# Performance work log

Measured on AMD Instinct MI355X. Metric: run time of the kernel, lower is better.

## Reference

```python
import jax, jax.numpy as jnp
import numpy as np

WIN = 9  # window size per spatial dim (default [9,9,9] for 3D)


def _window_sum(x):
    # Depthwise conv with an all-ones [9,9,9] kernel, stride 1, zero pad 4
    # == sliding-window box sum. lax.reduce_window is the efficient, exact form.
    pad = WIN // 2
    return jax.lax.reduce_window(
        x, 0.0, jax.lax.add,
        window_dimensions=(1, 1, WIN, WIN, WIN),
        window_strides=(1, 1, 1, 1, 1),
        padding=((0, 0), (0, 0), (pad, pad), (pad, pad), (pad, pad)),
    )


def setup_inputs() -> dict:
    key = jax.random.key(0)
    k1, k2 = jax.random.split(key)
    shape = (2, 1, 160, 160, 160)  # [B, C, D, H, W]
    y_true = jax.random.normal(k1, shape, dtype=jnp.float32)
    y_pred = jax.random.normal(k2, shape, dtype=jnp.float32)
    return {"y_true": y_true, "y_pred": y_pred}


def reference(y_true, y_pred):
    Ii, Ji = y_true, y_pred
    win_size = jnp.asarray(WIN ** 3, dtype=Ii.dtype)  # 729

    I2 = Ii * Ii
    J2 = Ji * Ji
    IJ = Ii * Ji

    I_sum = _window_sum(Ii)
    J_sum = _window_sum(Ji)
    I2_sum = _window_sum(I2)
    J2_sum = _window_sum(J2)
    IJ_sum = _window_sum(IJ)

    u_I = I_sum / win_size
    u_J = J_sum / win_size

    cross = IJ_sum - u_J * I_sum - u_I * J_sum + u_I * u_J * win_size
    I_var = I2_sum - 2.0 * u_I * I_sum + u_I * u_I * win_size
    J_var = J2_sum - 2.0 * u_J * J_sum + u_J * u_J * win_size

    cc = cross * cross / (I_var * J_var + 1e-05)
    # mean over spatial dims [2,3,4] -> [B,C], then mean -> scalar
    return (1.0 - jnp.mean(cc, axis=(2, 3, 4))).mean()
```

## Files before the change

### kernel.cpp

```cpp
#include <hip/hip_runtime.h>


typedef float floatx2 __attribute__((ext_vector_type(2)));

constexpr int W = 160, H = 160, D = 160;
constexpr int SLICE = W * H;
constexpr int NVOX  = W * H * D;
constexpr int BATCH = 2;
constexpr int FROW  = 5 * W;
constexpr float RW  = 1.0f / 729.0f;

constexpr int TPB_Z = 256;
constexpr int XG4   = W / 4;
constexpr int CHZ   = 8, NCHZ = D / CHZ;
constexpr int NTH_Z = BATCH * XG4 * H * NCHZ;
constexpr int NBLK_Z = NTH_Z / TPB_Z;

constexpr int TPB_YX = 256;
constexpr int XG  = W / 8;
constexpr int CHY = 4, NCHY = H / CHY;
constexpr int NTUP = BATCH * D * NCHY;
constexpr int TPW  = 3;
constexpr int TPBLK = 4 * TPW;
constexpr int NBLK_YX = (NTUP + TPBLK - 1) / TPBLK;

__device__ inline unsigned int pk4(float a, float b, float c, float d) {
    unsigned int u = 0;
    u = __builtin_amdgcn_cvt_pk_fp8_f32(a, b, u, false);
    u = __builtin_amdgcn_cvt_pk_fp8_f32(c, d, u, true);
    return u;
}
__device__ inline void up8(uint2 v, float* o) {
    floatx2 t;
    t = __builtin_amdgcn_cvt_pk_f32_fp8(v.x, false); o[0] = t[0]; o[1] = t[1];
    t = __builtin_amdgcn_cvt_pk_f32_fp8(v.x, true);  o[2] = t[0]; o[3] = t[1];
    t = __builtin_amdgcn_cvt_pk_f32_fp8(v.y, false); o[4] = t[0]; o[5] = t[1];
    t = __builtin_amdgcn_cvt_pk_f32_fp8(v.y, true);  o[6] = t[0]; o[7] = t[1];
}

__global__ __launch_bounds__(TPB_Z) void pass_z(const float* __restrict__ I,
                                                const float* __restrict__ J,
                                                unsigned char* __restrict__ outA) {
    int t = blockIdx.x * TPB_Z + threadIdx.x;
    int xg = t % XG4;
    int y  = (t / XG4) % H;
    int c  = (t / (XG4 * H)) % NCHZ;
    int b  = t / (XG4 * H * NCHZ);
    int x0 = xg * 4;
    const float* Ib = I + (size_t)b * NVOX + y * W + x0;
    const float* Jb = J + (size_t)b * NVOX + y * W + x0;
    unsigned char* ob = outA + ((size_t)b * D * H + y) * FROW + x0;

    float s[5][4];
#pragma unroll
    for (int f = 0; f < 5; ++f)
#pragma unroll
        for (int i = 0; i < 4; ++i) s[f][i] = 0.f;

    auto addS = [&](int zz) {
        float4 a = *(const float4*)(Ib + (size_t)zz * SLICE);
        float4 bb = *(const float4*)(Jb + (size_t)zz * SLICE);
        float av[4] = {a.x, a.y, a.z, a.w};
        float bv[4] = {bb.x, bb.y, bb.z, bb.w};
#pragma unroll
        for (int i = 0; i < 4; ++i) {
            float x = av[i], yv = bv[i];
            s[0][i] += x; s[1][i] += yv;
            s[2][i] += x * x; s[3][i] += yv * yv; s[4][i] += x * yv;
        }
    };

    int z0 = c * CHZ;
    for (int zz = (z0 - 4 < 0 ? 0 : z0 - 4); zz <= z0 + 4; ++zz) addS(zz);

#pragma unroll
    for (int dz = 0; dz < CHZ; ++dz) {
        int z = z0 + dz;
        int za = z + 5, zs = z - 4;
        bool ha = za < D, hs = zs >= 0;
        float4 Az = ha ? *(const float4*)(Ib + (size_t)za * SLICE) : make_float4(0.f, 0.f, 0.f, 0.f);
        float4 Bz = ha ? *(const float4*)(Jb + (size_t)za * SLICE) : make_float4(0.f, 0.f, 0.f, 0.f);
        float4 As = hs ? *(const float4*)(Ib + (size_t)zs * SLICE) : make_float4(0.f, 0.f, 0.f, 0.f);
        float4 Bs = hs ? *(const float4*)(Jb + (size_t)zs * SLICE) : make_float4(0.f, 0.f, 0.f, 0.f);

        unsigned char* op = ob + (size_t)z * (H * FROW);
#pragma unroll
        for (int f = 0; f < 5; ++f)
            *(unsigned int*)(op + f * W) = pk4(s[f][0], s[f][1], s[f][2], s[f][3]);

        float ae[4] = {Az.x, Az.y, Az.z, Az.w};
        float be[4] = {Bz.x, Bz.y, Bz.z, Bz.w};
        float al[4] = {As.x, As.y, As.z, As.w};
        float bl[4] = {Bs.x, Bs.y, Bs.z, Bs.w};
#pragma unroll
        for (int i = 0; i < 4; ++i) {
            s[0][i] += ae[i] - al[i];
            s[1][i] += be[i] - bl[i];
            s[2][i] += ae[i] * ae[i] - al[i] * al[i];
            s[3][i] += be[i] * be[i] - bl[i] * bl[i];
            s[4][i] += ae[i] * be[i] - al[i] * bl[i];
        }
    }
}

__global__ __launch_bounds__(TPB_YX) void pass_yx(const unsigned char* __restrict__ A,
                                                  double* __restrict__ partials) {
    int tid = threadIdx.x;
    int lane = tid & 63, wvi = tid >> 6;
    int g = lane / XG, xg = lane % XG;
    int tuple = blockIdx.x * TPBLK + wvi * TPW + g;
    bool valid = (g < TPW) && (tuple < NTUP);
    int t = valid ? tuple : 0;
    int yc = t % NCHY;
    int z  = (t / NCHY) % D;
    int b  = t / (NCHY * D);
    int x0 = xg * 8;
    const unsigned char* __restrict__ base =
        A + (size_t)(b * D + z) * H * FROW + x0;
    int y0 = yc * CHY;

    float s[5][8];
#pragma unroll
    for (int f = 0; f < 5; ++f)
#pragma unroll
        for (int i = 0; i < 8; ++i) s[f][i] = 0.f;

    int ylo = y0 - 4 < 0 ? 0 : y0 - 4;
    int yhi = y0 + 4 > H - 1 ? H - 1 : y0 + 4;
    for (int yy = ylo; yy <= yhi; ++yy) {
        const unsigned char* rp = base + (size_t)yy * FROW;
#pragma unroll
        for (int f = 0; f < 5; ++f) {
            uint2 v = *(const uint2*)(rp + f * W);
            float u[8]; up8(v, u);
#pragma unroll
            for (int i = 0; i < 8; ++i) s[f][i] += u[i];
        }
    }

    double acc = 0.0;
#pragma unroll
    for (int dy = 0; dy < CHY; ++dy) {
        int ye = y0 + dy + 5, yl = y0 + dy - 4;
        bool he = ye < H, hl = yl >= 0;
        uint2 pe[5], pl[5];
        const unsigned char* pre = base + (size_t)(he ? ye : 0) * FROW;
        const unsigned char* prl = base + (size_t)(hl ? yl : 0) * FROW;
#pragma unroll
        for (int f = 0; f < 5; ++f) {
            pe[f] = he ? *(const uint2*)(pre + f * W) : make_uint2(0u, 0u);
            pl[f] = hl ? *(const uint2*)(prl + f * W) : make_uint2(0u, 0u);
        }

        float wv5[5][8];
#pragma unroll
        for (int f = 0; f < 5; ++f) {
            float p0 = s[f][0];
            float p1 = p0 + s[f][1];
            float p2 = p1 + s[f][2];
            float p3 = p2 + s[f][3];
            float p4 = p3 + s[f][4];
            float p5 = p4 + s[f][5];
            float p6 = p5 + s[f][6];
            float tot = p6 + s[f][7];
            float a0 = tot - p3, a1 = tot - p4, a2 = tot - p5, a3 = tot - p6;
            float L0 = __shfl_up(a0, 1), L1 = __shfl_up(a1, 1);
            float L2 = __shfl_up(a2, 1), L3 = __shfl_up(a3, 1);
            float R0 = __shfl_down(p0, 1), R1 = __shfl_down(p1, 1);
            float R2 = __shfl_down(p2, 1), R3 = __shfl_down(p3, 1);
            if (xg == 0)      { L0 = 0.f; L1 = 0.f; L2 = 0.f; L3 = 0.f; }
            if (xg == XG - 1) { R0 = 0.f; R1 = 0.f; R2 = 0.f; R3 = 0.f; }
            wv5[f][0] = L0 + p4;
            wv5[f][1] = L1 + p5;
            wv5[f][2] = L2 + p6;
            wv5[f][3] = L3 + tot;
            wv5[f][4] = tot + R0;
            wv5[f][5] = (tot - p0) + R1;
            wv5[f][6] = (tot - p1) + R2;
            wv5[f][7] = (tot - p2) + R3;
        }

        float rowcc = 0.f;
#pragma unroll
        for (int i = 0; i < 8; ++i) {
            float Is = wv5[0][i], Js = wv5[1][i];
            float I2s = wv5[2][i], J2s = wv5[3][i], IJs = wv5[4][i];
            float tI = RW * Is;
            float cross = __builtin_fmaf(-tI, Js, IJs);
            float Iv    = __builtin_fmaf(-tI, Is, I2s);
            float Jv    = __builtin_fmaf(-(RW * Js), Js, J2s);
            float den   = __builtin_fmaf(Iv, Jv, 1e-5f);
            rowcc = __builtin_fmaf(cross * cross, __builtin_amdgcn_rcpf(den), rowcc);
        }
        acc += (double)rowcc;

#pragma unroll
        for (int f = 0; f < 5; ++f) {
            float ue[8], ul[8];
            up8(pe[f], ue); up8(pl[f], ul);
#pragma unroll
            for (int i = 0; i < 8; ++i) s[f][i] += ue[i] - ul[i];
        }
    }

    if (!valid) acc = 0.0;

#pragma unroll
    for (int off = 32; off > 0; off >>= 1) acc += __shfl_down(acc, off);
    __shared__ double sm[TPB_YX / 64];
    if ((tid & 63) == 0) sm[tid >> 6] = acc;
    __syncthreads();
    if (tid == 0) {
        double tt = 0.0;
#pragma unroll
        for (int i = 0; i < TPB_YX / 64; ++i) tt += sm[i];
        partials[blockIdx.x] = tt;
    }
}

__global__ __launch_bounds__(256) void finalize(const double* __restrict__ p,
                                                float* __restrict__ out) {
    double v = 0.0;
    for (int i = threadIdx.x; i < NBLK_YX; i += 256) v += p[i];
#pragma unroll
    for (int off = 32; off > 0; off >>= 1) v += __shfl_down(v, off);
    __shared__ double sm[4];
    int lane = threadIdx.x & 63, wid = threadIdx.x >> 6;
    if (lane == 0) sm[wid] = v;
    __syncthreads();
    if (threadIdx.x == 0) {
        double tt = 0.0;
#pragma unroll
        for (int i = 0; i < 4; ++i) tt += sm[i];
        out[0] = (float)(1.0 - tt / (double)((double)BATCH * (double)NVOX));
    }
}

extern "C" void kernel_launch(void* const* d_in, const int* in_sizes, int n_in,
                              void* d_out, int out_size, void* d_ws, size_t ws_size,
                              hipStream_t stream) {
    const float* I = (const float*)d_in[0];
    const float* J = (const float*)d_in[1];
    float* out = (float*)d_out;

    unsigned char* bufA = (unsigned char*)d_ws;
    double* partials = (double*)(bufA + ((size_t)BATCH * 5 * NVOX + 255) / 256 * 256);

    pass_z<<<NBLK_Z, TPB_Z, 0, stream>>>(I, J, bufA);
    pass_yx<<<NBLK_YX, TPB_YX, 0, stream>>>(bufA, partials);
    finalize<<<1, 256, 0, stream>>>(partials, out);
}
```

Before: 68.34 us.

## Move x-window sum into z pass and drop shuffles from y pass

The z pass now loads a 12-wide neighborhood (left, middle, right float4) for each thread, keeps z-running sums over 12 columns, and writes x-windowed sums to the fp8 intermediate. The y pass then only needs the y sliding window, so the cross-lane shuffles and prefix sums go away, and its chunk size drops from 4 to 2 with a simpler one-tuple-per-thread mapping. The aim is cheaper pass_y work and more parallelism. In exchange the z pass reads three times as much input per slice and holds three times as many accumulators, which raises register pressure. The z inner loop is also no longer unrolled.

```diff
diff --git a/kernel.cpp b/kernel.cpp
--- a/kernel.cpp
+++ b/kernel.cpp
@@ -11,18 +11,16 @@
 constexpr float RW  = 1.0f / 729.0f;
 
 constexpr int TPB_Z = 256;
-constexpr int XG4   = W / 4;
+constexpr int XGZ   = W / 4;
 constexpr int CHZ   = 8, NCHZ = D / CHZ;
-constexpr int NTH_Z = BATCH * XG4 * H * NCHZ;
+constexpr int NTH_Z = BATCH * XGZ * H * NCHZ;
 constexpr int NBLK_Z = NTH_Z / TPB_Z;
 
-constexpr int TPB_YX = 256;
-constexpr int XG  = W / 8;
-constexpr int CHY = 4, NCHY = H / CHY;
-constexpr int NTUP = BATCH * D * NCHY;
-constexpr int TPW  = 3;
-constexpr int TPBLK = 4 * TPW;
-constexpr int NBLK_YX = (NTUP + TPBLK - 1) / TPBLK;
+constexpr int TPB_Y = 256;
+constexpr int XGY   = W / 8;
+constexpr int CHY   = 2, NCHY = H / CHY;
+constexpr int NTH_Y = BATCH * D * NCHY * XGY;
+constexpr int NBLK_Y = NTH_Y / TPB_Y;
 
 __device__ inline unsigned int pk4(float a, float b, float c, float d) {
     unsigned int u = 0;
@@ -42,117 +40,63 @@
                                                 const float* __restrict__ J,
                                                 unsigned char* __restrict__ outA) {
     int t = blockIdx.x * TPB_Z + threadIdx.x;
-    int xg = t % XG4;
-    int y  = (t / XG4) % H;
-    int c  = (t / (XG4 * H)) % NCHZ;
-    int b  = t / (XG4 * H * NCHZ);
+    int xg = t % XGZ;
+    int y  = (t / XGZ) % H;
+    int c  = (t / (XGZ * H)) % NCHZ;
+    int b  = t / (XGZ * H * NCHZ);
     int x0 = xg * 4;
     const float* Ib = I + (size_t)b * NVOX + y * W + x0;
     const float* Jb = J + (size_t)b * NVOX + y * W + x0;
-    unsigned char* ob = outA + ((size_t)b * D * H + y) * FROW + x0;
-
-    float s[5][4];
+    bool hasL = xg > 0, hasR = xg < XGZ - 1;
+    const float4 Z4 = make_float4(0.f, 0.f, 0.f, 0.f);
+
+    float s[5][12];
 #pragma unroll
     for (int f = 0; f < 5; ++f)
 #pragma unroll
-        for (int i = 0; i < 4; ++i) s[f][i] = 0.f;
-
-    auto addS = [&](int zz) {
-        float4 a = *(const float4*)(Ib + (size_t)zz * SLICE);
-        float4 bb = *(const float4*)(Jb + (size_t)zz * SLICE);
-        float av[4] = {a.x, a.y, a.z, a.w};
-        float bv[4] = {bb.x, bb.y, bb.z, bb.w};
-#pragma unroll
-        for (int i = 0; i < 4; ++i) {
-            float x = av[i], yv = bv[i];
-            s[0][i] += x; s[1][i] += yv;
-            s[2][i] += x * x; s[3][i] += yv * yv; s[4][i] += x * yv;
+        for (int i = 0; i < 12; ++i) s[f][i] = 0.f;
+
+    auto addT = [&](int zz) {
+        const float* ip = Ib + (size_t)zz * SLICE;
+        const float* jp = Jb + (size_t)zz * SLICE;
+        float4 Li = hasL ? *(const float4*)(ip - 4) : Z4;
+        float4 Mi = *(const float4*)(ip);
+        float4 Ri = hasR ? *(const float4*)(ip + 4) : Z4;
+        float4 Lj = hasL ? *(const float4*)(jp - 4) : Z4;
+        float4 Mj = *(const float4*)(jp);
+        float4 Rj = hasR ? *(const float4*)(jp + 4) : Z4;
+        float a[12] = {Li.x, Li.y, Li.z, Li.w, Mi.x, Mi.y, Mi.z, Mi.w, Ri.x, Ri.y, Ri.z, Ri.w};
+        float bb[12] = {Lj.x, Lj.y, Lj.z, Lj.w, Mj.x, Mj.y, Mj.z, Mj.w, Rj.x, Rj.y, Rj.z, Rj.w};
+#pragma unroll
+        for (int i = 0; i < 12; ++i) {
+            s[0][i] += a[i]; s[1][i] += bb[i];
+            s[2][i] += a[i] * a[i]; s[3][i] += bb[i] * bb[i]; s[4][i] += a[i] * bb[i];
         }
     };
+    auto subT = [&](int zz) {
+        const float* ip = Ib + (size_t)zz * SLICE;
+        const float* jp = Jb + (size_t)zz * SLICE;
+        float4 Li = hasL ? *(const float4*)(ip - 4) : Z4;
+        float4 Mi = *(const float4*)(ip);
+        float4 Ri = hasR ? *(const float4*)(ip + 4) : Z4;
+        float4 Lj = hasL ? *(const float4*)(jp - 4) : Z4;
+        float4 Mj = *(const float4*)(jp);
+        float4 Rj = hasR ? *(const float4*)(jp + 4) : Z4;
+        float a[12] = {Li.x, Li.y, Li.z, Li.w, Mi.x, Mi.y, Mi.z, Mi.w, Ri.x, Ri.y, Ri.z, Ri.w};
+        float bb[12] = {Lj.x, Lj.y, Lj.z, Lj.w, Mj.x, Mj.y, Mj.z, Mj.w, Rj.x, Rj.y, Rj.z, Rj.w};
+#pragma unroll
+        for (int i = 0; i < 12; ++i) {
+            s[0][i] -= a[i]; s[1][i] -= bb[i];
+            s[2][i] -= a[i] * a[i]; s[3][i] -= bb[i] * bb[i]; s[4][i] -= a[i] * bb[i];
+        }
+    };
 
     int z0 = c * CHZ;
-    for (int zz = (z0 - 4 < 0 ? 0 : z0 - 4); zz <= z0 + 4; ++zz) addS(zz);
-
-#pragma unroll
+    for (int zz = (z0 - 4 < 0 ? 0 : z0 - 4); zz <= z0 + 4; ++zz) addT(zz);
+
     for (int dz = 0; dz < CHZ; ++dz) {
         int z = z0 + dz;
-        int za = z + 5, zs = z - 4;
-        bool ha = za < D, hs = zs >= 0;
-        float4 Az = ha ? *(const float4*)(Ib + (size_t)za * SLICE) : make_float4(0.f, 0.f, 0.f, 0.f);
-        float4 Bz = ha ? *(const float4*)(Jb + (size_t)za * SLICE) : make_float4(0.f, 0.f, 0.f, 0.f);
-        float4 As = hs ? *(const float4*)(Ib + (size_t)zs * SLICE) : make_float4(0.f, 0.f, 0.f, 0.f);
-        float4 Bs = hs ? *(const float4*)(Jb + (size_t)zs * SLICE) : make_float4(0.f, 0.f, 0.f, 0.f);
-
-        unsigned char* op = ob + (size_t)z * (H * FROW);
-#pragma unroll
-        for (int f = 0; f < 5; ++f)
-            *(unsigned int*)(op + f * W) = pk4(s[f][0], s[f][1], s[f][2], s[f][3]);
-
-        float ae[4] = {Az.x, Az.y, Az.z, Az.w};
-        float be[4] = {Bz.x, Bz.y, Bz.z, Bz.w};
-        float al[4] = {As.x, As.y, As.z, As.w};
-        float bl[4] = {Bs.x, Bs.y, Bs.z, Bs.w};
-#pragma unroll
-        for (int i = 0; i < 4; ++i) {
-            s[0][i] += ae[i] - al[i];
-            s[1][i] += be[i] - bl[i];
-            s[2][i] += ae[i] * ae[i] - al[i] * al[i];
-            s[3][i] += be[i] * be[i] - bl[i] * bl[i];
-            s[4][i] += ae[i] * be[i] - al[i] * bl[i];
-        }
-    }
-}
-
-__global__ __launch_bounds__(TPB_YX) void pass_yx(const unsigned char* __restrict__ A,
-                                                  double* __restrict__ partials) {
-    int tid = threadIdx.x;
-    int lane = tid & 63, wvi = tid >> 6;
-    int g = lane / XG, xg = lane % XG;
-    int tuple = blockIdx.x * TPBLK + wvi * TPW + g;
-    bool valid = (g < TPW) && (tuple < NTUP);
-    int t = valid ? tuple : 0;
-    int yc = t % NCHY;
-    int z  = (t / NCHY) % D;
-    int b  = t / (NCHY * D);
-    int x0 = xg * 8;
-    const unsigned char* __restrict__ base =
-        A + (size_t)(b * D + z) * H * FROW + x0;
-    int y0 = yc * CHY;
-
-    float s[5][8];
-#pragma unroll
-    for (int f = 0; f < 5; ++f)
-#pragma unroll
-        for (int i = 0; i < 8; ++i) s[f][i] = 0.f;
-
-    int ylo = y0 - 4 < 0 ? 0 : y0 - 4;
-    int yhi = y0 + 4 > H - 1 ? H - 1 : y0 + 4;
-    for (int yy = ylo; yy <= yhi; ++yy) {
-        const unsigned char* rp = base + (size_t)yy * FROW;
-#pragma unroll
-        for (int f = 0; f < 5; ++f) {
-            uint2 v = *(const uint2*)(rp + f * W);
-            float u[8]; up8(v, u);
-#pragma unroll
-            for (int i = 0; i < 8; ++i) s[f][i] += u[i];
-        }
-    }
-
-    double acc = 0.0;
-#pragma unroll
-    for (int dy = 0; dy < CHY; ++dy) {
-        int ye = y0 + dy + 5, yl = y0 + dy - 4;
-        bool he = ye < H, hl = yl >= 0;
-        uint2 pe[5], pl[5];
-        const unsigned char* pre = base + (size_t)(he ? ye : 0) * FROW;
-        const unsigned char* prl = base + (size_t)(hl ? yl : 0) * FROW;
-#pragma unroll
-        for (int f = 0; f < 5; ++f) {
-            pe[f] = he ? *(const uint2*)(pre + f * W) : make_uint2(0u, 0u);
-            pl[f] = hl ? *(const uint2*)(prl + f * W) : make_uint2(0u, 0u);
-        }
-
-        float wv5[5][8];
+        unsigned char* op = outA + ((size_t)(b * D + z) * H + y) * FROW + x0;
 #pragma unroll
         for (int f = 0; f < 5; ++f) {
             float p0 = s[f][0];
@@ -162,29 +106,71 @@
             float p4 = p3 + s[f][4];
             float p5 = p4 + s[f][5];
             float p6 = p5 + s[f][6];
-            float tot = p6 + s[f][7];
-            float a0 = tot - p3, a1 = tot - p4, a2 = tot - p5, a3 = tot - p6;
-            float L0 = __shfl_up(a0, 1), L1 = __shfl_up(a1, 1);
-            float L2 = __shfl_up(a2, 1), L3 = __shfl_up(a3, 1);
-            float R0 = __shfl_down(p0, 1), R1 = __shfl_down(p1, 1);
-            float R2 = __shfl_down(p2, 1), R3 = __shfl_down(p3, 1);
-            if (xg == 0)      { L0 = 0.f; L1 = 0.f; L2 = 0.f; L3 = 0.f; }
-            if (xg == XG - 1) { R0 = 0.f; R1 = 0.f; R2 = 0.f; R3 = 0.f; }
-            wv5[f][0] = L0 + p4;
-            wv5[f][1] = L1 + p5;
-            wv5[f][2] = L2 + p6;
-            wv5[f][3] = L3 + tot;
-            wv5[f][4] = tot + R0;
-            wv5[f][5] = (tot - p0) + R1;
-            wv5[f][6] = (tot - p1) + R2;
-            wv5[f][7] = (tot - p2) + R3;
+            float p7 = p6 + s[f][7];
+            float p8 = p7 + s[f][8];
+            float p9 = p8 + s[f][9];
+            float p10 = p9 + s[f][10];
+            float p11 = p10 + s[f][11];
+            *(unsigned int*)(op + f * W) = pk4(p8, p9 - p0, p10 - p1, p11 - p2);
+        }
+        int za = z + 5, zs = z - 4;
+        if (za < D) addT(za);
+        if (zs >= 0) subT(zs);
+    }
+}
+
+__global__ __launch_bounds__(TPB_Y) void pass_y(const unsigned char* __restrict__ A,
+                                                double* __restrict__ partials) {
+    int tid = threadIdx.x;
+    int t = blockIdx.x * TPB_Y + tid;
+    int xg = t % XGY;
+    int tup = t / XGY;
+    int yc = tup % NCHY;
+    int z  = (tup / NCHY) % D;
+    int b  = tup / (NCHY * D);
+    int x0 = xg * 8;
+    const unsigned char* __restrict__ base =
+        A + (size_t)(b * D + z) * H * FROW + x0;
+    int y0 = yc * CHY;
+
+    float s[5][8];
+#pragma unroll
+    for (int f = 0; f < 5; ++f)
+#pragma unroll
+        for (int i = 0; i < 8; ++i) s[f][i] = 0.f;
+
+    int ylo = y0 - 4 < 0 ? 0 : y0 - 4;
+    int yhi = y0 + 4 > H - 1 ? H - 1 : y0 + 4;
+    for (int yy = ylo; yy <= yhi; ++yy) {
+        const unsigned char* rp = base + (size_t)yy * FROW;
+#pragma unroll
+        for (int f = 0; f < 5; ++f) {
+            uint2 v = *(const uint2*)(rp + f * W);
+            float u[8]; up8(v, u);
+#pragma unroll
+            for (int i = 0; i < 8; ++i) s[f][i] += u[i];
+        }
+    }
+
+    double acc = 0.0;
+#pragma unroll
+    for (int dy = 0; dy < CHY; ++dy) {
+        int ye = y0 + dy + 5, yl = y0 + dy - 4;
+        bool he = ye < H, hl = yl >= 0;
+        uint2 pe[5], pl[5];
+        const unsigned char* pre = base + (size_t)(he ? ye : 0) * FROW;
+        const unsigned char* prl = base + (size_t)(hl ? yl : 0) * FROW;
+#pragma unroll
+        for (int f = 0; f < 5; ++f) {
+            pe[f] = he ? *(const uint2*)(pre + f * W) : make_uint2(0u, 0u);
+            pl[f] = hl ? *(const uint2*)(prl + f * W) : make_uint2(0u, 0u);
         }
 
         float rowcc = 0.f;
 #pragma unroll
         for (int i = 0; i < 8; ++i) {
-            float Is = wv5[0][i], Js = wv5[1][i];
-            float I2s = wv5[2][i], J2s = wv5[3][i], IJs = wv5[4][i];
+            float Is = s[0][i], Js = s[1][i];
+            float I2s = s[2][i], J2s = s[3][i], IJs = s[4][i];
             float tI = RW * Is;
             float cross = __builtin_fmaf(-tI, Js, IJs);
             float Iv    = __builtin_fmaf(-tI, Is, I2s);
@@ -203,17 +189,15 @@
         }
     }
 
-    if (!valid) acc = 0.0;
-
 #pragma unroll
     for (int off = 32; off > 0; off >>= 1) acc += __shfl_down(acc, off);
-    __shared__ double sm[TPB_YX / 64];
+    __shared__ double sm[TPB_Y / 64];
     if ((tid & 63) == 0) sm[tid >> 6] = acc;
     __syncthreads();
     if (tid == 0) {
         double tt = 0.0;
 #pragma unroll
-        for (int i = 0; i < TPB_YX / 64; ++i) tt += sm[i];
+        for (int i = 0; i < TPB_Y / 64; ++i) tt += sm[i];
         partials[blockIdx.x] = tt;
     }
 }
@@ -221,7 +205,7 @@
 __global__ __launch_bounds__(256) void finalize(const double* __restrict__ p,
                                                 float* __restrict__ out) {
     double v = 0.0;
-    for (int i = threadIdx.x; i < NBLK_YX; i += 256) v += p[i];
+    for (int i = threadIdx.x; i < NBLK_Y; i += 256) v += p[i];
 #pragma unroll
     for (int off = 32; off > 0; off >>= 1) v += __shfl_down(v, off);
     __shared__ double sm[4];
@@ -247,6 +231,6 @@
     double* partials = (double*)(bufA + ((size_t)BATCH * 5 * NVOX + 255) / 256 * 256);
 
     pass_z<<<NBLK_Z, TPB_Z, 0, stream>>>(I, J, bufA);
-    pass_yx<<<NBLK_YX, TPB_YX, 0, stream>>>(bufA, partials);
+    pass_y<<<NBLK_Y, TPB_Y, 0, stream>>>(bufA, partials);
     finalize<<<1, 256, 0, stream>>>(partials, out);
 }
```

Measured after the change: 124.9 us. 82.7% more time.

## Split fused yx pass into separate x-box-sum and y-sliding passes

Applied to the files above, without the earlier changes.

The combined y/x pass is split into a standalone x-direction box-sum kernel that writes an intermediate fp8 buffer, followed by a y-direction sliding-sum kernel that computes the NCC terms. This removes the per-row shuffle-based x prefix sums from the y loop and the wasted idle lanes of the old tuple mapping, and the y chunk is shortened to 2 rows for more threads. In exchange it adds a full extra read and write of the 5-field fp8 volume, an extra kernel launch, and a second fp8 quantization of the x sums, which may cost accuracy.

```diff
diff --git a/kernel.cpp b/kernel.cpp
--- a/kernel.cpp
+++ b/kernel.cpp
@@ -11,18 +11,20 @@
 constexpr float RW  = 1.0f / 729.0f;
 
 constexpr int TPB_Z = 256;
-constexpr int XG4   = W / 4;
+constexpr int XGZ   = W / 4;
 constexpr int CHZ   = 8, NCHZ = D / CHZ;
-constexpr int NTH_Z = BATCH * XG4 * H * NCHZ;
+constexpr int NTH_Z = BATCH * XGZ * H * NCHZ;
 constexpr int NBLK_Z = NTH_Z / TPB_Z;
 
-constexpr int TPB_YX = 256;
-constexpr int XG  = W / 8;
-constexpr int CHY = 4, NCHY = H / CHY;
-constexpr int NTUP = BATCH * D * NCHY;
-constexpr int TPW  = 3;
-constexpr int TPBLK = 4 * TPW;
-constexpr int NBLK_YX = (NTUP + TPBLK - 1) / TPBLK;
+constexpr int TPB_X = 256;
+constexpr int XGY   = W / 8;
+constexpr int NTH_X = BATCH * D * H * XGY;
+constexpr int NBLK_X = NTH_X / TPB_X;
+
+constexpr int TPB_Y = 256;
+constexpr int CHY   = 2, NCHY = H / CHY;
+constexpr int NTH_Y = BATCH * D * NCHY * XGY;
+constexpr int NBLK_Y = NTH_Y / TPB_Y;
 
 __device__ inline unsigned int pk4(float a, float b, float c, float d) {
     unsigned int u = 0;
@@ -42,10 +44,10 @@
                                                 const float* __restrict__ J,
                                                 unsigned char* __restrict__ outA) {
     int t = blockIdx.x * TPB_Z + threadIdx.x;
-    int xg = t % XG4;
-    int y  = (t / XG4) % H;
-    int c  = (t / (XG4 * H)) % NCHZ;
-    int b  = t / (XG4 * H * NCHZ);
+    int xg = t % XGZ;
+    int y  = (t / XGZ) % H;
+    int c  = (t / (XGZ * H)) % NCHZ;
+    int b  = t / (XGZ * H * NCHZ);
     int x0 = xg * 4;
     const float* Ib = I + (size_t)b * NVOX + y * W + x0;
     const float* Jb = J + (size_t)b * NVOX + y * W + x0;
@@ -103,17 +105,46 @@
     }
 }
 
-__global__ __launch_bounds__(TPB_YX) void pass_yx(const unsigned char* __restrict__ A,
-                                                  double* __restrict__ partials) {
+__global__ __launch_bounds__(TPB_X) void pass_x(const unsigned char* __restrict__ A,
+                                                unsigned char* __restrict__ B) {
+    int t = blockIdx.x * TPB_X + threadIdx.x;
+    int xg = t % XGY;
+    int row = t / XGY;
+    int x0 = xg * 8;
+    const unsigned char* rp = A + (size_t)row * FROW + x0;
+    unsigned char* op = B + (size_t)row * FROW + x0;
+    bool hasL = xg > 0, hasR = xg < XGY - 1;
+
+#pragma unroll
+    for (int f = 0; f < 5; ++f) {
+        uint2 cl = hasL ? *(const uint2*)(rp + f * W - 8) : make_uint2(0u, 0u);
+        uint2 cc = *(const uint2*)(rp + f * W);
+        uint2 cr = hasR ? *(const uint2*)(rp + f * W + 8) : make_uint2(0u, 0u);
+        float v[24];
+        up8(cl, v); up8(cc, v + 8); up8(cr, v + 16);
+        float P[24];
+        P[0] = v[0];
+#pragma unroll
+        for (int k = 1; k < 24; ++k) P[k] = P[k - 1] + v[k];
+        float o[8];
+#pragma unroll
+        for (int i = 0; i < 8; ++i) o[i] = P[i + 12] - P[i + 3];
+        uint2 w;
+        w.x = pk4(o[0], o[1], o[2], o[3]);
+        w.y = pk4(o[4], o[5], o[6], o[7]);
+        *(uint2*)(op + f * W) = w;
+    }
+}
+
+__global__ __launch_bounds__(TPB_Y) void pass_y(const unsigned char* __restrict__ A,
+                                                double* __restrict__ partials) {
     int tid = threadIdx.x;
-    int lane = tid & 63, wvi = tid >> 6;
-    int g = lane / XG, xg = lane % XG;
-    int tuple = blockIdx.x * TPBLK + wvi * TPW + g;
-    bool valid = (g < TPW) && (tuple < NTUP);
-    int t = valid ? tuple : 0;
-    int yc = t % NCHY;
-    int z  = (t / NCHY) % D;
-    int b  = t / (NCHY * D);
+    int t = blockIdx.x * TPB_Y + tid;
+    int xg = t % XGY;
+    int tup = t / XGY;
+    int yc = tup % NCHY;
+    int z  = (tup / NCHY) % D;
+    int b  = tup / (NCHY * D);
     int x0 = xg * 8;
     const unsigned char* __restrict__ base =
         A + (size_t)(b * D + z) * H * FROW + x0;
@@ -152,39 +183,11 @@
             pl[f] = hl ? *(const uint2*)(prl + f * W) : make_uint2(0u, 0u);
         }
 
-        float wv5[5][8];
-#pragma unroll
-        for (int f = 0; f < 5; ++f) {
-            float p0 = s[f][0];
-            float p1 = p0 + s[f][1];
-            float p2 = p1 + s[f][2];
-            float p3 = p2 + s[f][3];
-            float p4 = p3 + s[f][4];
-            float p5 = p4 + s[f][5];
-            float p6 = p5 + s[f][6];
-            float tot = p6 + s[f][7];
-            float a0 = tot - p3, a1 = tot - p4, a2 = tot - p5, a3 = tot - p6;
-            float L0 = __shfl_up(a0, 1), L1 = __shfl_up(a1, 1);
-            float L2 = __shfl_up(a2, 1), L3 = __shfl_up(a3, 1);
-            float R0 = __shfl_down(p0, 1), R1 = __shfl_down(p1, 1);
-            float R2 = __shfl_down(p2, 1), R3 = __shfl_down(p3, 1);
-            if (xg == 0)      { L0 = 0.f; L1 = 0.f; L2 = 0.f; L3 = 0.f; }
-            if (xg == XG - 1) { R0 = 0.f; R1 = 0.f; R2 = 0.f; R3 = 0.f; }
-            wv5[f][0] = L0 + p4;
-            wv5[f][1] = L1 + p5;
-            wv5[f][2] = L2 + p6;
-            wv5[f][3] = L3 + tot;
-            wv5[f][4] = tot + R0;
-            wv5[f][5] = (tot - p0) + R1;
-            wv5[f][6] = (tot - p1) + R2;
-            wv5[f][7] = (tot - p2) + R3;
-        }
-
         float rowcc = 0.f;
 #pragma unroll
         for (int i = 0; i < 8; ++i) {
-            float Is = wv5[0][i], Js = wv5[1][i];
-            float I2s = wv5[2][i], J2s = wv5[3][i], IJs = wv5[4][i];
+            float Is = s[0][i], Js = s[1][i];
+            float I2s = s[2][i], J2s = s[3][i], IJs = s[4][i];
             float tI = RW * Is;
             float cross = __builtin_fmaf(-tI, Js, IJs);
             float Iv    = __builtin_fmaf(-tI, Is, I2s);
@@ -203,17 +206,15 @@
         }
     }
 
-    if (!valid) acc = 0.0;
-
 #pragma unroll
     for (int off = 32; off > 0; off >>= 1) acc += __shfl_down(acc, off);
-    __shared__ double sm[TPB_YX / 64];
+    __shared__ double sm[TPB_Y / 64];
     if ((tid & 63) == 0) sm[tid >> 6] = acc;
     __syncthreads();
     if (tid == 0) {
         double tt = 0.0;
 #pragma unroll
-        for (int i = 0; i < TPB_YX / 64; ++i) tt += sm[i];
+        for (int i = 0; i < TPB_Y / 64; ++i) tt += sm[i];
         partials[blockIdx.x] = tt;
     }
 }
@@ -221,7 +222,7 @@
 __global__ __launch_bounds__(256) void finalize(const double* __restrict__ p,
                                                 float* __restrict__ out) {
     double v = 0.0;
-    for (int i = threadIdx.x; i < NBLK_YX; i += 256) v += p[i];
+    for (int i = threadIdx.x; i < NBLK_Y; i += 256) v += p[i];
 #pragma unroll
     for (int off = 32; off > 0; off >>= 1) v += __shfl_down(v, off);
     __shared__ double sm[4];
@@ -243,10 +244,13 @@
     const float* J = (const float*)d_in[1];
     float* out = (float*)d_out;
 
+    size_t bufsz = ((size_t)BATCH * 5 * NVOX + 255) / 256 * 256;
     unsigned char* bufA = (unsigned char*)d_ws;
-    double* partials = (double*)(bufA + ((size_t)BATCH * 5 * NVOX + 255) / 256 * 256);
+    unsigned char* bufB = bufA + bufsz;
+    double* partials = (double*)(bufB + bufsz);
 
     pass_z<<<NBLK_Z, TPB_Z, 0, stream>>>(I, J, bufA);
-    pass_yx<<<NBLK_YX, TPB_YX, 0, stream>>>(bufA, partials);
+    pass_x<<<NBLK_X, TPB_X, 0, stream>>>(bufA, bufB);
+    pass_y<<<NBLK_Y, TPB_Y, 0, stream>>>(bufB, partials);
     finalize<<<1, 256, 0, stream>>>(partials, out);
 }
```

Result: slower. 76.42 us (+11.8%).
